# Performance work log

Measured on AMD Instinct MI355X. Metric: run time of the kernel, lower is better.

## Reference

```python
import jax, jax.numpy as jnp
import numpy as np

BEV = 128          # bev_res
EMBED = 128        # embed_dim
HEADS = 8
POINTS = 4
HD = EMBED // HEADS  # head dim = 16


def setup_inputs() -> dict:
    key = jax.random.key(0)
    ks = jax.random.split(key, 9)
    bs, nq = 4, BEV * BEV
    s = lambda k, shape: jax.random.normal(k, shape, jnp.float32) * 0.02
    return {
        "query": jax.random.normal(ks[0], (bs, nq, EMBED), jnp.float32),
        "W_off": s(ks[1], (EMBED, HEADS * POINTS * 2)),
        "b_off": s(ks[2], (HEADS * POINTS * 2,)),
        "W_attn": s(ks[3], (EMBED, HEADS * POINTS)),
        "b_attn": s(ks[4], (HEADS * POINTS,)),
        "W_val": s(ks[5], (EMBED, EMBED)),
        "b_val": s(ks[6], (EMBED,)),
        "W_out": s(ks[7], (EMBED, EMBED)),
        "b_out": s(ks[8], (EMBED,)),
    }


def _ref_points():
    # matches np.meshgrid(linspace(0,1,BEV), linspace(0,1,BEV), indexing='ij');
    # stacked as (col, row) = (x, y), flattened row-major to (BEV*BEV, 2)
    lin = jnp.linspace(0.0, 1.0, BEV)
    gy, gx = jnp.meshgrid(lin, lin, indexing="ij")
    return jnp.stack([gx, gy], axis=-1).reshape(-1, 2)


def _msda(query, W_off, b_off, W_attn, b_attn, W_val, b_val, W_out, b_out):
    bs, nq, _ = query.shape
    H = W = BEV
    # value projection; single level so num_value == nq == H*W
    value = query @ W_val + b_val
    v = value.reshape(bs, nq, HEADS, HD).transpose(0, 2, 1, 3)  # (bs, heads, HW, hd)

    # sampling offsets and attention weights (softmax over levels*points = points)
    off = (query @ W_off + b_off).reshape(bs, nq, HEADS, POINTS, 2)
    aw = jax.nn.softmax((query @ W_attn + b_attn).reshape(bs, nq, HEADS, POINTS), axis=-1)

    ref = _ref_points()  # (nq, 2) in [0,1], (x, y)
    norm = jnp.array([W, H], jnp.float32)  # offset_normalizer = (W, H)
    loc = ref[None, :, None, None, :] + off / norm  # (bs, nq, heads, pts, 2)

    # grid_sample bilinear, align_corners=False, padding_mode='zeros'
    px = loc[..., 0] * W - 0.5
    py = loc[..., 1] * H - 0.5
    x0 = jnp.floor(px)
    y0 = jnp.floor(py)
    wx = px - x0  # weight toward x0+1
    wy = py - y0
    x0i = x0.astype(jnp.int32)
    y0i = y0.astype(jnp.int32)

    def flat(a):  # (bs, nq, heads, pts) -> (bs, heads, nq*pts)
        return a.transpose(0, 2, 1, 3).reshape(bs, HEADS, nq * POINTS)

    def samp(xi, yi):
        valid = ((xi >= 0) & (xi < W) & (yi >= 0) & (yi < H)).astype(v.dtype)
        xc = jnp.clip(xi, 0, W - 1)
        yc = jnp.clip(yi, 0, H - 1)
        idx = flat(yc * W + xc)  # (bs, heads, nq*pts)
        g = jnp.take_along_axis(v, idx[..., None], axis=2)  # (bs, heads, nq*pts, hd)
        return g * flat(valid)[..., None]

    s00 = samp(x0i, y0i)
    s01 = samp(x0i + 1, y0i)
    s10 = samp(x0i, y0i + 1)
    s11 = samp(x0i + 1, y0i + 1)
    wxf = flat(wx)[..., None]
    wyf = flat(wy)[..., None]
    sampled = (s00 * (1 - wxf) * (1 - wyf) + s01 * wxf * (1 - wyf)
               + s10 * (1 - wxf) * wyf + s11 * wxf * wyf)
    sampled = sampled.reshape(bs, HEADS, nq, POINTS, HD)

    awt = aw.transpose(0, 2, 1, 3)  # (bs, heads, nq, pts)
    out = jnp.einsum("bhnpd,bhnp->bnhd", sampled, awt).reshape(bs, nq, EMBED)
    out = out @ W_out + b_out
    # mmcv MSDA adds identity (=query) internally; SelfAttention adds residual again
    return out + 2.0 * query


def reference(query, W_off, b_off, W_attn, b_attn, W_val, b_val, W_out, b_out):
    return _msda(query, W_off, b_off, W_attn, b_attn, W_val, b_val, W_out, b_out)
```

## Files before the change

kernel.cpp:

```cpp
#include <hip/hip_runtime.h>

#define BS 4
#define NQ 16384
#define GTOK 65536

typedef unsigned short u16;
typedef unsigned int u32;
typedef __attribute__((ext_vector_type(8))) short bf16x8;
typedef __attribute__((ext_vector_type(4))) short bf16x4;
typedef __attribute__((ext_vector_type(4))) float f32x4;
typedef __attribute__((ext_vector_type(2))) float f32x2;
typedef __attribute__((ext_vector_type(4))) unsigned int u32x4;

__device__ __forceinline__ float bf2f(u16 v) { return __uint_as_float(((u32)v) << 16); }
__device__ __forceinline__ u16 f2bf(float f) {
    u32 u = __float_as_uint(f);
    u32 r = (u + 0x7fffu + ((u >> 16) & 1u)) >> 16;
    return (u16)r;
}
__device__ __forceinline__ u32 pk2bf(float lo, float hi) {
    return (u32)f2bf(lo) | ((u32)f2bf(hi) << 16);
}
__device__ __forceinline__ bf16x8 make_afrag(const float* qrow) {
    f32x4 q0 = *(const f32x4*)(qrow);
    f32x4 q1 = *(const f32x4*)(qrow + 4);
    union { bf16x8 v; u32 u[4]; } a;
    a.u[0] = pk2bf(q0.x, q0.y); a.u[1] = pk2bf(q0.z, q0.w);
    a.u[2] = pk2bf(q1.x, q1.y); a.u[3] = pk2bf(q1.z, q1.w);
    return a.v;
}

__global__ __launch_bounds__(256)
void setup_kernel(const float* __restrict__ W_val, const float* __restrict__ W_off,
                  const float* __restrict__ W_attn, const float* __restrict__ W_out,
                  u16* __restrict__ Wswz, u16* __restrict__ Wout_swz)
{
    const int i = blockIdx.x * 256 + threadIdx.x;
    if (i < 28672) {
        const int j = i & 7, lane = (i >> 3) & 15, quad = (i >> 7) & 3;
        const int kb = (i >> 9) & 3, nt = i >> 11;
        const int k = kb * 32 + quad * 8 + j;
        const int n = nt * 16 + lane;
        float v;
        if (n < 128)      v = W_val[k * 128 + n];
        else if (n < 192) v = W_off[k * 64 + (n - 128)];
        else              v = W_attn[k * 32 + (n - 192)];
        Wswz[i] = f2bf(v);
    } else if (i < 45056) {
        const int i2 = i - 28672;
        const int j = i2 & 7, lane = (i2 >> 3) & 15, quad = (i2 >> 7) & 3;
        const int kb = (i2 >> 9) & 3, nt = i2 >> 11;
        const int k = kb * 32 + quad * 8 + j;
        const int n = nt * 16 + lane;
        Wout_swz[i2] = f2bf(W_out[k * 128 + n]);
    }
}

__global__ __launch_bounds__(256)
void prepass_kernel(const float* __restrict__ query,
                    const float* __restrict__ b_off, const float* __restrict__ b_attn,
                    const float* __restrict__ b_val,
                    const u16* __restrict__ Wswz,
                    u16* __restrict__ val, u16* __restrict__ offattn)
{
    __shared__ __align__(16) u16 stage[64 * 136];
    const int tid = threadIdx.x;
    const int w = tid >> 6, l = tid & 63;
    const int lane16 = l & 15, quad = l >> 4;
    const int gtok0 = blockIdx.x * 64;
    const bf16x8* Wf = (const bf16x8*)Wswz;

    const int tl = w * 16 + lane16;
    const float* qrow = query + (size_t)(gtok0 + tl) * 128 + quad * 8;
    bf16x8 afrag[4];
    #pragma unroll
    for (int kb = 0; kb < 4; ++kb)
        afrag[kb] = make_afrag(qrow + kb * 32);

    #pragma unroll
    for (int nt = 0; nt < 8; ++nt) {
        f32x4 acc = {0.f, 0.f, 0.f, 0.f};
        const bf16x8* bp = Wf + ((size_t)(nt * 4) * 4 + quad) * 16 + lane16;
        #pragma unroll
        for (int kb = 0; kb < 4; ++kb)
            acc = __builtin_amdgcn_mfma_f32_16x16x32_bf16(afrag[kb], bp[kb * 64], acc, 0, 0, 0);
        const float bias = b_val[nt * 16 + lane16];
        #pragma unroll
        for (int r = 0; r < 4; ++r)
            stage[(w * 16 + quad * 4 + r) * 136 + nt * 16 + lane16] = f2bf(acc[r] + bias);
    }
    f32x4 oacc[6];
    #pragma unroll
    for (int j = 0; j < 6; ++j) {
        const int nt = 8 + j;
        f32x4 acc = {0.f, 0.f, 0.f, 0.f};
        const bf16x8* bp = Wf + ((size_t)(nt * 4) * 4 + quad) * 16 + lane16;
        #pragma unroll
        for (int kb = 0; kb < 4; ++kb)
            acc = __builtin_amdgcn_mfma_f32_16x16x32_bf16(afrag[kb], bp[kb * 64], acc, 0, 0, 0);
        oacc[j] = acc;
    }
    __syncthreads();
    #pragma unroll
    for (int i = 0; i < 4; ++i) {
        const int chunk = i * 256 + tid;
        const int t = chunk >> 4, c16 = chunk & 15;
        u32x4 v = *(const u32x4*)&stage[t * 136 + c16 * 8];
        *(u32x4*)&val[(size_t)(gtok0 + t) * 128 + c16 * 8] = v;
    }
    __syncthreads();
    #pragma unroll
    for (int j = 0; j < 6; ++j) {
        const int c = j * 16 + lane16;
        const float bias = (c < 64) ? b_off[c] : b_attn[c - 64];
        #pragma unroll
        for (int r = 0; r < 4; ++r)
            stage[(w * 16 + quad * 4 + r) * 104 + c] = f2bf(oacc[j][r] + bias);
    }
    __syncthreads();
    #pragma unroll
    for (int i = 0; i < 3; ++i) {
        const int chunk = i * 256 + tid;
        const int t = chunk / 12, cj = chunk - t * 12;
        u32x4 v = *(const u32x4*)&stage[t * 104 + cj * 8];
        *(u32x4*)&offattn[(size_t)(gtok0 + t) * 96 + cj * 8] = v;
    }
}

__global__ __launch_bounds__(256, 3)
void fused_kernel(const float* __restrict__ query,
                  const float* __restrict__ b_out,
                  const u16* __restrict__ Wout_swz,
                  const u16* __restrict__ val, const u16* __restrict__ offattn,
                  float* __restrict__ out)
{
    __shared__ __align__(16) u16 vhalo[121 * 136];
    __shared__ __align__(16) u16 scratch[64 * 136];

    const int tid = threadIdx.x;
    const int bid = blockIdx.x;
    const int b_  = bid >> 8;
    const int sq  = bid & 255;
    const int Y   = (sq >> 4) * 8;
    const int X   = (sq & 15) * 8;
    const int HOX = X - 2 + (X >> 6);
    const int HOY = Y - 2 + (Y >> 6);

    const int w = tid >> 6, l = tid & 63;
    const int lane16 = l & 15, quad = l >> 4;
    const size_t batch_base = (size_t)b_ * NQ;

    const bf16x8* WfO = (const bf16x8*)Wout_swz;

    #pragma unroll
    for (int i = 0; i < 3; ++i) {
        const int chunk = i * 256 + tid;
        const int t = chunk / 12, cj = chunk - t * 12;
        const size_t gt = batch_base + (size_t)(Y + (t >> 3)) * 128 + (X + (t & 7));
        u32x4 v = *(const u32x4*)&offattn[gt * 96 + cj * 8];
        *(u32x4*)&scratch[t * 96 + cj * 8] = v;
    }
    #pragma unroll
    for (int i = 0; i < 8; ++i) {
        const int chunk = i * 256 + tid;
        if (chunk < 1936) {
            const int hp = chunk >> 4, c16 = chunk & 15;
            const int hy = hp / 11, hx = hp - hy * 11;
            const int gy = min(max(HOY + hy, 0), 127);
            const int gx = min(max(HOX + hx, 0), 127);
            const size_t gt = batch_base + (size_t)gy * 128 + gx;
            u32x4 v = *(const u32x4*)&val[gt * 128 + c16 * 8];
            const int col = ((((c16 >> 1) + hp) & 7) << 4) + ((c16 & 1) << 3);
            *(u32x4*)&vhalo[hp * 136 + col] = v;
        }
    }
    __syncthreads();

    float aw[2][4], ox[2][4], oy[2][4];
    #pragma unroll
    for (int it = 0; it < 2; ++it) {
        const int item = it * 256 + tid;
        const int t = item >> 3, h = item & 7;
        bf16x8 ofr = *(const bf16x8*)&scratch[t * 96 + h * 8];
        bf16x4 atr = *(const bf16x4*)&scratch[t * 96 + 64 + h * 4];
        #pragma unroll
        for (int p = 0; p < 4; ++p) {
            ox[it][p] = bf2f((u16)ofr[2 * p]);
            oy[it][p] = bf2f((u16)ofr[2 * p + 1]);
        }
        const float l0 = bf2f((u16)atr[0]), l1 = bf2f((u16)atr[1]);
        const float l2 = bf2f((u16)atr[2]), l3 = bf2f((u16)atr[3]);
        const float m = fmaxf(fmaxf(l0, l1), fmaxf(l2, l3));
        const float e0 = __expf(l0 - m), e1 = __expf(l1 - m);
        const float e2 = __expf(l2 - m), e3 = __expf(l3 - m);
        const float inv = 1.0f / (e0 + e1 + e2 + e3);
        aw[it][0] = e0 * inv; aw[it][1] = e1 * inv;
        aw[it][2] = e2 * inv; aw[it][3] = e3 * inv;
    }
    __syncthreads();

    #pragma unroll
    for (int it = 0; it < 2; ++it) {
        const int item = it * 256 + tid;
        const int t = item >> 3, h = item & 7;
        const int qx = X + (t & 7), qy = Y + (t >> 3);
        const float cx = (float)qx * (128.0f / 127.0f);
        const float cy = (float)qy * (128.0f / 127.0f);

        f32x2 acc2[8];
        #pragma unroll
        for (int d = 0; d < 8; ++d) acc2[d] = (f32x2){0.f, 0.f};

        #pragma unroll
        for (int p = 0; p < 4; ++p) {
            const float px = cx + ox[it][p] - 0.5f;
            const float py = cy + oy[it][p] - 0.5f;
            const float fx = floorf(px), fy = floorf(py);
            const float wx = px - fx, wy = py - fy;
            const int xi = (int)fx, yi = (int)fy;
            const float cw[4] = {(1.f - wx) * (1.f - wy), wx * (1.f - wy),
                                 (1.f - wx) * wy,         wx * wy};
            const int hx0 = min(max(xi - HOX, 0), 10), hx1 = min(hx0 + 1, 10);
            const int hy0 = min(max(yi - HOY, 0), 10), hy1 = min(hy0 + 1, 10);
            const int cxs[4] = {hx0, hx1, hx0, hx1};
            const int cys[4] = {hy0, hy0, hy1, hy1};
            const int gxs[4] = {xi, xi + 1, xi, xi + 1};
            const int gys[4] = {yi, yi, yi + 1, yi + 1};
            #pragma unroll
            for (int c4 = 0; c4 < 4; ++c4) {
                const bool valid = (gxs[c4] >= 0) & (gxs[c4] < 128) &
                                   (gys[c4] >= 0) & (gys[c4] < 128);
                const float wgt = valid ? cw[c4] * aw[it][p] : 0.f;
                const int hp = cys[c4] * 11 + cxs[c4];
                const int col = (((h + hp) & 7)) * 16;
                const u32* vp = (const u32*)&vhalo[hp * 136 + col];
                u32x4 ra = *(const u32x4*)vp;
                u32x4 rb = *(const u32x4*)(vp + 4);
                const f32x2 w2 = {wgt, wgt};
                #pragma unroll
                for (int d = 0; d < 4; ++d) {
                    const u32 da = ra[d];
                    f32x2 v = {__uint_as_float(da << 16),
                               __uint_as_float(da & 0xffff0000u)};
                    acc2[d] += w2 * v;
                }
                #pragma unroll
                for (int d = 0; d < 4; ++d) {
                    const u32 db = rb[d];
                    f32x2 v = {__uint_as_float(db << 16),
                               __uint_as_float(db & 0xffff0000u)};
                    acc2[4 + d] += w2 * v;
                }
            }
        }
        u32x4 s0, s1;
        #pragma unroll
        for (int d = 0; d < 4; ++d) {
            s0[d] = pk2bf(acc2[d].x, acc2[d].y);
            s1[d] = pk2bf(acc2[4 + d].x, acc2[4 + d].y);
        }
        *(u32x4*)&scratch[t * 136 + h * 16]     = s0;
        *(u32x4*)&scratch[t * 136 + h * 16 + 8] = s1;
    }
    __syncthreads();

    float* ostage = (float*)vhalo;
    {
        bf16x8 afrag[4];
        #pragma unroll
        for (int kb = 0; kb < 4; ++kb)
            afrag[kb] = *(const bf16x8*)&scratch[(w * 16 + lane16) * 136 + kb * 32 + quad * 8];

        #pragma unroll
        for (int nt = 0; nt < 8; ++nt) {
            f32x4 acc = {0.f, 0.f, 0.f, 0.f};
            const bf16x8* bp = WfO + ((size_t)(nt * 4) * 4 + quad) * 16 + lane16;
            #pragma unroll
            for (int kb = 0; kb < 4; ++kb)
                acc = __builtin_amdgcn_mfma_f32_16x16x32_bf16(afrag[kb], bp[kb * 64], acc, 0, 0, 0);
            const int n = nt * 16 + lane16;
            const float bias = b_out[n];
            const int pcol = ((((n >> 2) + 2 * quad) & 31) << 2) + (n & 3);
            #pragma unroll
            for (int r = 0; r < 4; ++r)
                ostage[(w * 16 + quad * 4 + r) * 128 + pcol] = acc[r] + bias;
        }
    }
    __syncthreads();
    #pragma unroll
    for (int i = 0; i < 8; ++i) {
        const int tok = w * 16 + 2 * i + (l >> 5);
        const int p = l & 31;
        const int c = (p - 2 * ((i >> 1) & 3)) & 31;
        f32x4 s = *(const f32x4*)&ostage[tok * 128 + p * 4];
        const size_t g = (batch_base + (size_t)(Y + (tok >> 3)) * 128 + (X + (tok & 7))) * 128
                         + (size_t)(c * 4);
        f32x4 q = *(const f32x4*)&query[g];
        f32x4 o;
        o.x = s.x + 2.0f * q.x; o.y = s.y + 2.0f * q.y;
        o.z = s.z + 2.0f * q.z; o.w = s.w + 2.0f * q.w;
        *(f32x4*)&out[g] = o;
    }
}

__global__ __launch_bounds__(256, 2)
void fused_legacy(const float* __restrict__ query,
                  const float* __restrict__ b_off, const float* __restrict__ b_attn,
                  const float* __restrict__ b_val, const float* __restrict__ b_out,
                  const u16* __restrict__ Wswz, const u16* __restrict__ Wout_swz,
                  float* __restrict__ out)
{
    __shared__ __align__(16) u16 vhalo[121 * 136];
    __shared__ __align__(16) u16 scratch[64 * 136 + 2048];

    const int tid = threadIdx.x;
    const int bid = blockIdx.x;
    const int b_  = bid >> 8;
    const int sq  = bid & 255;
    const int Y   = (sq >> 4) * 8;
    const int X   = (sq & 15) * 8;
    const int HOX = X - 2 + (X >> 6);
    const int HOY = Y - 2 + (Y >> 6);

    const int w = tid >> 6, l = tid & 63;
    const int lane16 = l & 15, quad = l >> 4;
    const size_t batch_base = (size_t)b_ * NQ;

    const bf16x8* Wf  = (const bf16x8*)Wswz;
    const bf16x8* WfO = (const bf16x8*)Wout_swz;

    {
        const int tl = w * 16 + lane16;
        const int ty = tl >> 3, tx = tl & 7;
        const size_t grow = batch_base + (size_t)(Y + ty) * 128 + (X + tx);
        const float* qrow = query + grow * 128 + quad * 8;
        bf16x8 afrag[4];
        #pragma unroll
        for (int kb = 0; kb < 4; ++kb)
            afrag[kb] = make_afrag(qrow + kb * 32);
        #pragma unroll
        for (int nt = 8; nt < 14; ++nt) {
            f32x4 acc = {0.f, 0.f, 0.f, 0.f};
            const bf16x8* bp = Wf + ((size_t)(nt * 4) * 4 + quad) * 16 + lane16;
            #pragma unroll
            for (int kb = 0; kb < 4; ++kb)
                acc = __builtin_amdgcn_mfma_f32_16x16x32_bf16(afrag[kb], bp[kb * 64], acc, 0, 0, 0);
            if (nt < 12) {
                const int c = (nt - 8) * 16 + lane16;
                const float bias = b_off[c];
                #pragma unroll
                for (int r = 0; r < 4; ++r)
                    scratch[(w * 16 + quad * 4 + r) * 96 + c] = f2bf(acc[r] + bias);
            } else {
                const int c = (nt - 12) * 16 + lane16;
                const float bias = b_attn[c];
                #pragma unroll
                for (int r = 0; r < 4; ++r)
                    scratch[(w * 16 + quad * 4 + r) * 96 + 64 + c] = f2bf(acc[r] + bias);
            }
        }
    }
    #pragma unroll
    for (int i = 0; i < 2; ++i) {
        const int a = w + 4 * i;
        int hp = a * 16 + lane16; if (hp > 120) hp = 120;
        const int hy = hp / 11, hx = hp - hy * 11;
        const int gy = min(max(HOY + hy, 0), 127);
        const int gx = min(max(HOX + hx, 0), 127);
        const float* qrow = query + (batch_base + (size_t)gy * 128 + gx) * 128 + quad * 8;
        bf16x8 afrag[4];
        #pragma unroll
        for (int kb = 0; kb < 4; ++kb)
            afrag[kb] = make_afrag(qrow + kb * 32);
        #pragma unroll
        for (int nt = 0; nt < 8; ++nt) {
            f32x4 acc = {0.f, 0.f, 0.f, 0.f};
            const bf16x8* bp = Wf + ((size_t)(nt * 4) * 4 + quad) * 16 + lane16;
            #pragma unroll
            for (int kb = 0; kb < 4; ++kb)
                acc = __builtin_amdgcn_mfma_f32_16x16x32_bf16(afrag[kb], bp[kb * 64], acc, 0, 0, 0);
            const float bias = b_val[nt * 16 + lane16];
            #pragma unroll
            for (int r = 0; r < 4; ++r) {
                int hpr = a * 16 + quad * 4 + r; if (hpr > 120) hpr = 120;
                const int col = ((nt + hpr) & 7) * 16 + lane16;
                vhalo[hpr * 136 + col] = f2bf(acc[r] + bias);
            }
        }
    }
    __syncthreads();

    float aw[2][4], ox[2][4], oy[2][4];
    #pragma unroll
    for (int it = 0; it < 2; ++it) {
        const int item = it * 256 + tid;
        const int t = item >> 3, h = item & 7;
        bf16x8 ofr = *(const bf16x8*)&scratch[t * 96 + h * 8];
        bf16x4 atr = *(const bf16x4*)&scratch[t * 96 + 64 + h * 4];
        #pragma unroll
        for (int p = 0; p < 4; ++p) {
            ox[it][p] = bf2f((u16)ofr[2 * p]);
            oy[it][p] = bf2f((u16)ofr[2 * p + 1]);
        }
        const float l0 = bf2f((u16)atr[0]), l1 = bf2f((u16)atr[1]);
        const float l2 = bf2f((u16)atr[2]), l3 = bf2f((u16)atr[3]);
        const float m = fmaxf(fmaxf(l0, l1), fmaxf(l2, l3));
        const float e0 = __expf(l0 - m), e1 = __expf(l1 - m);
        const float e2 = __expf(l2 - m), e3 = __expf(l3 - m);
        const float inv = 1.0f / (e0 + e1 + e2 + e3);
        aw[it][0] = e0 * inv; aw[it][1] = e1 * inv;
        aw[it][2] = e2 * inv; aw[it][3] = e3 * inv;
    }
    __syncthreads();

    #pragma unroll
    for (int it = 0; it < 2; ++it) {
        const int item = it * 256 + tid;
        const int t = item >> 3, h = item & 7;
        const int qx = X + (t & 7), qy = Y + (t >> 3);
        const float cx = (float)qx * (128.0f / 127.0f);
        const float cy = (float)qy * (128.0f / 127.0f);

        f32x2 acc2[8];
        #pragma unroll
        for (int d = 0; d < 8; ++d) acc2[d] = (f32x2){0.f, 0.f};

        #pragma unroll
        for (int p = 0; p < 4; ++p) {
            const float px = cx + ox[it][p] - 0.5f;
            const float py = cy + oy[it][p] - 0.5f;
            const float fx = floorf(px), fy = floorf(py);
            const float wx = px - fx, wy = py - fy;
            const int xi = (int)fx, yi = (int)fy;
            const float cw[4] = {(1.f - wx) * (1.f - wy), wx * (1.f - wy),
                                 (1.f - wx) * wy,         wx * wy};
            const int hx0 = min(max(xi - HOX, 0), 10), hx1 = min(hx0 + 1, 10);
            const int hy0 = min(max(yi - HOY, 0), 10), hy1 = min(hy0 + 1, 10);
            const int cxs[4] = {hx0, hx1, hx0, hx1};
            const int cys[4] = {hy0, hy0, hy1, hy1};
            const int gxs[4] = {xi, xi + 1, xi, xi + 1};
            const int gys[4] = {yi, yi, yi + 1, yi + 1};
            #pragma unroll
            for (int c4 = 0; c4 < 4; ++c4) {
                const bool valid = (gxs[c4] >= 0) & (gxs[c4] < 128) &
                                   (gys[c4] >= 0) & (gys[c4] < 128);
                const float wgt = valid ? cw[c4] * aw[it][p] : 0.f;
                const int hp = cys[c4] * 11 + cxs[c4];
                const int col = (((h + hp) & 7)) * 16;
                const u32* vp = (const u32*)&vhalo[hp * 136 + col];
                u32x4 ra = *(const u32x4*)vp;
                u32x4 rb = *(const u32x4*)(vp + 4);
                const f32x2 w2 = {wgt, wgt};
                #pragma unroll
                for (int d = 0; d < 4; ++d) {
                    const u32 da = ra[d];
                    f32x2 v = {__uint_as_float(da << 16),
                               __uint_as_float(da & 0xffff0000u)};
                    acc2[d] += w2 * v;
                }
                #pragma unroll
                for (int d = 0; d < 4; ++d) {
                    const u32 db = rb[d];
                    f32x2 v = {__uint_as_float(db << 16),
                               __uint_as_float(db & 0xffff0000u)};
                    acc2[4 + d] += w2 * v;
                }
            }
        }
        u32x4 s0, s1;
        #pragma unroll
        for (int d = 0; d < 4; ++d) {
            s0[d] = pk2bf(acc2[d].x, acc2[d].y);
            s1[d] = pk2bf(acc2[4 + d].x, acc2[4 + d].y);
        }
        *(u32x4*)&scratch[t * 136 + h * 16]     = s0;
        *(u32x4*)&scratch[t * 136 + h * 16 + 8] = s1;
    }
    __syncthreads();

    float* ostage = (float*)vhalo;
    {
        bf16x8 afrag[4];
        #pragma unroll
        for (int kb = 0; kb < 4; ++kb)
            afrag[kb] = *(const bf16x8*)&scratch[(w * 16 + lane16) * 136 + kb * 32 + quad * 8];

        #pragma unroll
        for (int nt = 0; nt < 8; ++nt) {
            f32x4 acc = {0.f, 0.f, 0.f, 0.f};
            const bf16x8* bp = WfO + ((size_t)(nt * 4) * 4 + quad) * 16 + lane16;
            #pragma unroll
            for (int kb = 0; kb < 4; ++kb)
                acc = __builtin_amdgcn_mfma_f32_16x16x32_bf16(afrag[kb], bp[kb * 64], acc, 0, 0, 0);
            const int n = nt * 16 + lane16;
            const float bias = b_out[n];
            const int pcol = ((((n >> 2) + 2 * quad) & 31) << 2) + (n & 3);
            #pragma unroll
            for (int r = 0; r < 4; ++r)
                ostage[(w * 16 + quad * 4 + r) * 128 + pcol] = acc[r] + bias;
        }
    }
    __syncthreads();
    #pragma unroll
    for (int i = 0; i < 8; ++i) {
        const int tok = w * 16 + 2 * i + (l >> 5);
        const int p = l & 31;
        const int c = (p - 2 * ((i >> 1) & 3)) & 31;
        f32x4 s = *(const f32x4*)&ostage[tok * 128 + p * 4];
        const size_t g = (batch_base + (size_t)(Y + (tok >> 3)) * 128 + (X + (tok & 7))) * 128
                         + (size_t)(c * 4);
        f32x4 q = *(const f32x4*)&query[g];
        f32x4 o;
        o.x = s.x + 2.0f * q.x; o.y = s.y + 2.0f * q.y;
        o.z = s.z + 2.0f * q.z; o.w = s.w + 2.0f * q.w;
        *(f32x4*)&out[g] = o;
    }
}

extern "C" void kernel_launch(void* const* d_in, const int* in_sizes, int n_in,
                              void* d_out, int out_size, void* d_ws, size_t ws_size,
                              hipStream_t stream)
{
    const float* query  = (const float*)d_in[0];
    const float* W_off  = (const float*)d_in[1];
    const float* b_off  = (const float*)d_in[2];
    const float* W_attn = (const float*)d_in[3];
    const float* b_attn = (const float*)d_in[4];
    const float* W_val  = (const float*)d_in[5];
    const float* b_val  = (const float*)d_in[6];
    const float* W_out  = (const float*)d_in[7];
    const float* b_out  = (const float*)d_in[8];
    float* out = (float*)d_out;

    u16* Wswz     = (u16*)d_ws;
    u16* Wout_swz = (u16*)((char*)d_ws + 57344);

    const size_t OFF_VAL = 131072;
    const size_t OFF_OA  = OFF_VAL + (size_t)GTOK * 128 * 2;
    const size_t WS_NEED = OFF_OA + (size_t)GTOK * 96 * 2;

    setup_kernel<<<176, 256, 0, stream>>>(W_val, W_off, W_attn, W_out, Wswz, Wout_swz);

    if (ws_size >= WS_NEED) {
        u16* val = (u16*)((char*)d_ws + OFF_VAL);
        u16* oa  = (u16*)((char*)d_ws + OFF_OA);
        prepass_kernel<<<1024, 256, 0, stream>>>(query, b_off, b_attn, b_val,
                                                 Wswz, val, oa);
        fused_kernel<<<1024, 256, 0, stream>>>(query, b_out, Wout_swz, val, oa, out);
    } else {
        fused_legacy<<<1024, 256, 0, stream>>>(query, b_off, b_attn, b_val, b_out,
                                               Wswz, Wout_swz, out);
    }
}
```

Before: 129.7 us.

## Compute offset/attention projection inside fused kernel instead of prepass

The offset and attention-logit projection moves out of the prepass into the fused sampling kernel. Each block now computes it with MFMA directly from the query rows of its 8x8 tile and writes the result to shared scratch. This removes the global write and re-read of the 96-channel offattn buffer and shrinks the workspace. The cost is extra MFMA work and query reads inside the fused kernel, plus more register pressure under its occupancy bound of 3 blocks.

Result: no change. 132.0 us (+1.8%).

```diff
diff --git a/kernel.cpp b/kernel.cpp
--- a/kernel.cpp
+++ b/kernel.cpp
@@ -58,10 +58,9 @@
 
 __global__ __launch_bounds__(256)
 void prepass_kernel(const float* __restrict__ query,
-                    const float* __restrict__ b_off, const float* __restrict__ b_attn,
                     const float* __restrict__ b_val,
                     const u16* __restrict__ Wswz,
-                    u16* __restrict__ val, u16* __restrict__ offattn)
+                    u16* __restrict__ val)
 {
     __shared__ __align__(16) u16 stage[64 * 136];
     const int tid = threadIdx.x;
@@ -89,17 +88,6 @@
         for (int r = 0; r < 4; ++r)
             stage[(w * 16 + quad * 4 + r) * 136 + nt * 16 + lane16] = f2bf(acc[r] + bias);
     }
-    f32x4 oacc[6];
-    #pragma unroll
-    for (int j = 0; j < 6; ++j) {
-        const int nt = 8 + j;
-        f32x4 acc = {0.f, 0.f, 0.f, 0.f};
-        const bf16x8* bp = Wf + ((size_t)(nt * 4) * 4 + quad) * 16 + lane16;
-        #pragma unroll
-        for (int kb = 0; kb < 4; ++kb)
-            acc = __builtin_amdgcn_mfma_f32_16x16x32_bf16(afrag[kb], bp[kb * 64], acc, 0, 0, 0);
-        oacc[j] = acc;
-    }
     __syncthreads();
     #pragma unroll
     for (int i = 0; i < 4; ++i) {
@@ -108,30 +96,14 @@
         u32x4 v = *(const u32x4*)&stage[t * 136 + c16 * 8];
         *(u32x4*)&val[(size_t)(gtok0 + t) * 128 + c16 * 8] = v;
     }
-    __syncthreads();
-    #pragma unroll
-    for (int j = 0; j < 6; ++j) {
-        const int c = j * 16 + lane16;
-        const float bias = (c < 64) ? b_off[c] : b_attn[c - 64];
-        #pragma unroll
-        for (int r = 0; r < 4; ++r)
-            stage[(w * 16 + quad * 4 + r) * 104 + c] = f2bf(oacc[j][r] + bias);
-    }
-    __syncthreads();
-    #pragma unroll
-    for (int i = 0; i < 3; ++i) {
-        const int chunk = i * 256 + tid;
-        const int t = chunk / 12, cj = chunk - t * 12;
-        u32x4 v = *(const u32x4*)&stage[t * 104 + cj * 8];
-        *(u32x4*)&offattn[(size_t)(gtok0 + t) * 96 + cj * 8] = v;
-    }
 }
 
 __global__ __launch_bounds__(256, 3)
 void fused_kernel(const float* __restrict__ query,
+                  const float* __restrict__ b_off, const float* __restrict__ b_attn,
                   const float* __restrict__ b_out,
-                  const u16* __restrict__ Wout_swz,
-                  const u16* __restrict__ val, const u16* __restrict__ offattn,
+                  const u16* __restrict__ Wswz, const u16* __restrict__ Wout_swz,
+                  const u16* __restrict__ val,
                   float* __restrict__ out)
 {
     __shared__ __align__(16) u16 vhalo[121 * 136];
@@ -150,16 +122,9 @@
     const int lane16 = l & 15, quad = l >> 4;
     const size_t batch_base = (size_t)b_ * NQ;
 
+    const bf16x8* Wf  = (const bf16x8*)Wswz;
     const bf16x8* WfO = (const bf16x8*)Wout_swz;
 
-    #pragma unroll
-    for (int i = 0; i < 3; ++i) {
-        const int chunk = i * 256 + tid;
-        const int t = chunk / 12, cj = chunk - t * 12;
-        const size_t gt = batch_base + (size_t)(Y + (t >> 3)) * 128 + (X + (t & 7));
-        u32x4 v = *(const u32x4*)&offattn[gt * 96 + cj * 8];
-        *(u32x4*)&scratch[t * 96 + cj * 8] = v;
-    }
     #pragma unroll
     for (int i = 0; i < 8; ++i) {
         const int chunk = i * 256 + tid;
@@ -172,6 +137,37 @@
             u32x4 v = *(const u32x4*)&val[gt * 128 + c16 * 8];
             const int col = ((((c16 >> 1) + hp) & 7) << 4) + ((c16 & 1) << 3);
             *(u32x4*)&vhalo[hp * 136 + col] = v;
+        }
+    }
+    {
+        const int tl = w * 16 + lane16;
+        const int ty = tl >> 3, tx = tl & 7;
+        const size_t grow = batch_base + (size_t)(Y + ty) * 128 + (X + tx);
+        const float* qrow = query + grow * 128 + quad * 8;
+        bf16x8 afrag[4];
+        #pragma unroll
+        for (int kb = 0; kb < 4; ++kb)
+            afrag[kb] = make_afrag(qrow + kb * 32);
+        #pragma unroll
+        for (int nt = 8; nt < 14; ++nt) {
+            f32x4 acc = {0.f, 0.f, 0.f, 0.f};
+            const bf16x8* bp = Wf + ((size_t)(nt * 4) * 4 + quad) * 16 + lane16;
+            #pragma unroll
+            for (int kb = 0; kb < 4; ++kb)
+                acc = __builtin_amdgcn_mfma_f32_16x16x32_bf16(afrag[kb], bp[kb * 64], acc, 0, 0, 0);
+            if (nt < 12) {
+                const int c = (nt - 8) * 16 + lane16;
+                const float bias = b_off[c];
+                #pragma unroll
+                for (int r = 0; r < 4; ++r)
+                    scratch[(w * 16 + quad * 4 + r) * 96 + c] = f2bf(acc[r] + bias);
+            } else {
+                const int c = (nt - 12) * 16 + lane16;
+                const float bias = b_attn[c];
+                #pragma unroll
+                for (int r = 0; r < 4; ++r)
+                    scratch[(w * 16 + quad * 4 + r) * 96 + 64 + c] = f2bf(acc[r] + bias);
+            }
         }
     }
     __syncthreads();
@@ -536,17 +532,15 @@
     u16* Wout_swz = (u16*)((char*)d_ws + 57344);
 
     const size_t OFF_VAL = 131072;
-    const size_t OFF_OA  = OFF_VAL + (size_t)GTOK * 128 * 2;
-    const size_t WS_NEED = OFF_OA + (size_t)GTOK * 96 * 2;
+    const size_t WS_NEED = OFF_VAL + (size_t)GTOK * 128 * 2;
 
     setup_kernel<<<176, 256, 0, stream>>>(W_val, W_off, W_attn, W_out, Wswz, Wout_swz);
 
     if (ws_size >= WS_NEED) {
         u16* val = (u16*)((char*)d_ws + OFF_VAL);
-        u16* oa  = (u16*)((char*)d_ws + OFF_OA);
-        prepass_kernel<<<1024, 256, 0, stream>>>(query, b_off, b_attn, b_val,
-                                                 Wswz, val, oa);
-        fused_kernel<<<1024, 256, 0, stream>>>(query, b_out, Wout_swz, val, oa, out);
+        prepass_kernel<<<1024, 256, 0, stream>>>(query, b_val, Wswz, val);
+        fused_kernel<<<1024, 256, 0, stream>>>(query, b_off, b_attn, b_out,
+                                               Wswz, Wout_swz, val, out);
     } else {
         fused_legacy<<<1024, 256, 0, stream>>>(query, b_off, b_attn, b_val, b_out,
                                                Wswz, Wout_swz, out);
```
